# Performance work log

Hardware: AMD Instinct MI355X
Metric: run time of the kernel (lower is better)

## Reference

```python
import jax, jax.numpy as jnp
import numpy as np

E = 1024  # embed_dim
H = 16    # num_heads
D = E // H  # head_dim
B, S = 2, 2048


def setup_inputs() -> dict:
    key = jax.random.key(0)
    ks = jax.random.split(key, 8)
    q = jax.random.normal(ks[0], (B, S, E), dtype=jnp.float32)
    k = jax.random.normal(ks[1], (B, S, E), dtype=jnp.float32)
    v = jax.random.normal(ks[2], (B, S, E), dtype=jnp.float32)
    mask = jax.random.randint(ks[3], (1, 1, S, S), 0, 2, dtype=jnp.int32)
    sc = 1.0 / np.sqrt(E)
    Wqkv = jax.random.normal(ks[4], (E, 3 * E), dtype=jnp.float32) * sc  # [in, out]
    bqkv = jnp.zeros((3 * E,), dtype=jnp.float32)
    Wout = jax.random.normal(ks[5], (E, E), dtype=jnp.float32) * sc
    bout = jnp.zeros((E,), dtype=jnp.float32)
    return {"q": q, "k": k, "v": v, "mask": mask,
            "Wqkv": Wqkv, "bqkv": bqkv, "Wout": Wout, "bout": bout}


def reference(q, k, v, mask, Wqkv, bqkv, Wout, bout):
    # Fused QKV projection: project cat([q,k,v], dim=0) with the shared 3E proj,
    # then take the Q slice for q, K slice for k, V slice for v.
    x = jnp.concatenate([q, k, v], axis=0)            # [3B, S, E]
    full = jnp.einsum('bse,ef->bsf', x, Wqkv) + bqkv  # [3B, S, 3E]
    qf, kf, vf = jnp.split(full, 3, axis=0)           # each [B, S, 3E]
    qh = qf[..., :E].reshape(B, S, H, D).transpose(0, 2, 1, 3)       # [B,H,S,D]
    kh = kf[..., E:2 * E].reshape(B, S, H, D).transpose(0, 2, 1, 3)
    vh = vf[..., 2 * E:].reshape(B, S, H, D).transpose(0, 2, 1, 3)
    scores = jnp.einsum('bhqd,bhkd->bhqk', qh, kh) / np.sqrt(D)      # [B,H,S,S]
    scores = jnp.where(mask == 0, -jnp.inf, scores)
    attn = jax.nn.softmax(scores, axis=-1)
    ctx = jnp.einsum('bhqk,bhkd->bhqd', attn, vh)                    # [B,H,S,D]
    ctx = ctx.transpose(0, 2, 1, 3).reshape(B, S, E)
    return jnp.einsum('bse,ef->bsf', ctx, Wout) + bout
```

## Files before the change

kernel.cpp:

```cpp
#include <hip/hip_runtime.h>
#include <stdint.h>

#define EDIM 1024
#define HNUM 16
#define HD   64
#define BB   2
#define SS   2048
#define MTOT (BB * SS)

typedef __attribute__((ext_vector_type(8))) __bf16 bf16x8;
typedef __attribute__((ext_vector_type(8))) short short8;
typedef __attribute__((ext_vector_type(4))) short short4v;
typedef __attribute__((ext_vector_type(4))) float f32x4;

__device__ __forceinline__ short f2bf(float f) {
  union { float f; unsigned u; } x{f};
  unsigned r = (x.u + 0x7FFFu + ((x.u >> 16) & 1u)) >> 16;
  return (short)r;
}

__device__ __forceinline__ void gload16(const void* g, void* l) {
  __builtin_amdgcn_global_load_lds((const __attribute__((address_space(1))) void*)g,
                                   (__attribute__((address_space(3))) void*)l, 16, 0, 0);
}

__global__ __launch_bounds__(256) void cast_bf16(const float* __restrict__ s,
                                                 short* __restrict__ d, int n8) {
  int i = blockIdx.x * 256 + threadIdx.x;
  if (i >= n8) return;
  const float4* sp = (const float4*)s + (size_t)i * 2;
  float4 a = sp[0], b = sp[1];
  short8 r;
  r[0] = f2bf(a.x); r[1] = f2bf(a.y); r[2] = f2bf(a.z); r[3] = f2bf(a.w);
  r[4] = f2bf(b.x); r[5] = f2bf(b.y); r[6] = f2bf(b.z); r[7] = f2bf(b.w);
  *(short8*)(d + (size_t)i * 8) = r;
}

__global__ __launch_bounds__(256) void tcast(const float* __restrict__ W, int ld,
                                             int col0, short* __restrict__ D) {
  __shared__ short L[64][80];
  const int t = threadIdx.x;
  const int k0 = blockIdx.x * 64, n0 = blockIdx.y * 64;
  {
    const int kr = t >> 2, nc0 = (t & 3) * 16;
    #pragma unroll
    for (int u = 0; u < 4; ++u) {
      float4 f = *(const float4*)(W + (size_t)(k0 + kr) * ld + col0 + n0 + nc0 + u * 4);
      L[nc0 + u * 4 + 0][kr] = f2bf(f.x);
      L[nc0 + u * 4 + 1][kr] = f2bf(f.y);
      L[nc0 + u * 4 + 2][kr] = f2bf(f.z);
      L[nc0 + u * 4 + 3][kr] = f2bf(f.w);
    }
  }
  __syncthreads();
  {
    const int nr = t >> 2, kc = (t & 3) * 16;
    #pragma unroll
    for (int u = 0; u < 2; ++u) {
      short8 v = *(const short8*)&L[nr][kc + u * 8];
      *(short8*)(D + (size_t)(n0 + nr) * EDIM + k0 + kc + u * 8) = v;
    }
  }
}

__global__ __launch_bounds__(256) void pack_mask(const int* __restrict__ mask,
                                                 unsigned long long* __restrict__ pm) {
  const int wid = (blockIdx.x * 256 + threadIdx.x) >> 6;
  const int lane = threadIdx.x & 63;
  const int q = wid >> 5, kt = wid & 31;
  const int m = mask[(size_t)q * SS + kt * 64 + lane];
  const unsigned long long b = __ballot(m != 0);
  if (lane == 0) pm[(size_t)q * 32 + kt] = b;
}

template <int NFR, typename OT>
__device__ __forceinline__ void gemm_body(
    const short* __restrict__ A, const short* __restrict__ Bt,
    const float* __restrict__ bias, OT* __restrict__ O,
    int m0, int n0, int K, int N, float scale, short* As, short* Bs) {
  const int t = threadIdx.x;
  const int w = t >> 6, l = t & 63;
  const int wr = w >> 1, wc = w & 1;
  const int lr4 = l >> 4, lc = l & 15;

  f32x4 acc[4][NFR] = {};
  const int srow = t >> 3;
  const int schunk = (t & 7) ^ (srow & 7);

  for (int k0 = 0; k0 < K; k0 += 64) {
    #pragma unroll
    for (int p = 0; p < 4; ++p)
      gload16(A + (size_t)(m0 + 32 * p + srow) * K + k0 + schunk * 8,
              As + p * 2048 + w * 512);
    #pragma unroll
    for (int p = 0; p < NFR; ++p)
      gload16(Bt + (size_t)(n0 + 32 * p + srow) * K + k0 + schunk * 8,
              Bs + p * 2048 + w * 512);
    __syncthreads();

    #pragma unroll
    for (int kf = 0; kf < 2; ++kf) {
      const int c = ((4 * kf + lr4) ^ (lc & 7)) * 8;
      bf16x8 a[4], bfr[NFR];
      #pragma unroll
      for (int i = 0; i < 4; ++i)
        a[i] = *(const bf16x8*)(As + (64 * wr + 16 * i + lc) * 64 + c);
      #pragma unroll
      for (int j = 0; j < NFR; ++j)
        bfr[j] = *(const bf16x8*)(Bs + (16 * NFR * wc + 16 * j + lc) * 64 + c);
      #pragma unroll
      for (int i = 0; i < 4; ++i)
        #pragma unroll
        for (int j = 0; j < NFR; ++j)
          acc[i][j] = __builtin_amdgcn_mfma_f32_16x16x32_bf16(a[i], bfr[j], acc[i][j], 0, 0, 0);
    }
    __syncthreads();
  }

  #pragma unroll
  for (int j = 0; j < NFR; ++j) {
    const int col = n0 + 16 * NFR * wc + 16 * j + lc;
    const float bv = bias[col - n0 + n0];
    #pragma unroll
    for (int i = 0; i < 4; ++i) {
      const int rbase = m0 + 64 * wr + 16 * i + 4 * lr4;
      #pragma unroll
      for (int r = 0; r < 4; ++r) {
        float v = (acc[i][j][r] + bv) * scale;
        if constexpr (__is_same(OT, short))
          O[(size_t)(rbase + r) * N + col] = f2bf(v);
        else
          O[(size_t)(rbase + r) * N + col] = v;
      }
    }
  }
}

__global__ __launch_bounds__(256) void gemm_qkv(
    const short* __restrict__ Qb, const short* __restrict__ Kb,
    const short* __restrict__ Vb, const short* __restrict__ WqT,
    const short* __restrict__ WkT, const short* __restrict__ WvT,
    const float* __restrict__ bqkv, short* __restrict__ Qpj,
    short* __restrict__ Kpj, short* __restrict__ Vpj) {
  __shared__ short As[128 * 64];
  __shared__ short Bs[128 * 64];
  const int sel = blockIdx.y >> 3;
  const int n0 = (blockIdx.y & 7) * 128;
  const short* A  = sel == 0 ? Qb : (sel == 1 ? Kb : Vb);
  const short* Bt = sel == 0 ? WqT : (sel == 1 ? WkT : WvT);
  short* O = sel == 0 ? Qpj : (sel == 1 ? Kpj : Vpj);
  const float scale = sel == 0 ? 0.125f : 1.0f;
  gemm_body<4, short>(A, Bt, bqkv + (sel << 10), O, blockIdx.x * 128, n0,
                      EDIM, EDIM, scale, As, Bs);
}

__global__ __launch_bounds__(256) void gemm_out(
    const short* __restrict__ A, const short* __restrict__ Bt,
    const float* __restrict__ bias, float* __restrict__ O) {
  __shared__ short As[128 * 64];
  __shared__ short Bs[64 * 64];
  gemm_body<2, float>(A, Bt, bias, O, blockIdx.x * 128, blockIdx.y * 64,
                      EDIM, EDIM, 1.0f, As, Bs);
}

__global__ __launch_bounds__(256) void attn_mfma(
    const short* __restrict__ Qp, const short* __restrict__ Kp,
    const short* __restrict__ Vp, const unsigned long long* __restrict__ pmask,
    short* __restrict__ Ctx) {
  __shared__ short Ks[2][64 * 64];
  __shared__ short Vt[2][64 * 64];

  const int t = threadIdx.x, w = t >> 6, l = t & 63;
  const int lr4 = l >> 4, lc = l & 15;
  const int q0 = blockIdx.x * 64;
  const int h = blockIdx.y, b = blockIdx.z;
  const size_t hb = (size_t)b * SS * EDIM + (size_t)h * HD;
  const int qrow = q0 + 16 * w + lc;

  bf16x8 qf[2];
  #pragma unroll
  for (int kf = 0; kf < 2; ++kf)
    qf[kf] = *(const bf16x8*)(Qp + hb + (size_t)qrow * EDIM + 32 * kf + 8 * lr4);

  const int srow = t >> 3;
  const int schunk = (t & 7) ^ (srow & 7);
  const int vkey = t & 63;
  const int vdg = (t >> 6) * 16;
  const int kap = (vkey & 0x20) | ((vkey & 0xC) << 1) | ((vkey & 0x10) >> 2) | (vkey & 3);
  const int kapc = kap >> 3, kapb = kap & 7;

  #pragma unroll
  for (int p = 0; p < 2; ++p)
    gload16(Kp + hb + (size_t)(32 * p + srow) * EDIM + schunk * 8,
            &Ks[0][p * 2048 + w * 512]);
  {
    short8 v0 = *(const short8*)(Vp + hb + (size_t)vkey * EDIM + vdg);
    short8 v1 = *(const short8*)(Vp + hb + (size_t)vkey * EDIM + vdg + 8);
    #pragma unroll
    for (int e = 0; e < 8; ++e) {
      const int d0 = vdg + e, d1 = vdg + 8 + e;
      Vt[0][d0 * 64 + ((kapc ^ (d0 & 7)) << 3) + kapb] = v0[e];
      Vt[0][d1 * 64 + ((kapc ^ (d1 & 7)) << 3) + kapb] = v1[e];
    }
  }
  __syncthreads();

  f32x4 accO[4] = {};
  float mrow = -1e30f, lrow = 0.f;
  const int NT = SS / 64;

  for (int kt = 0; kt < NT; ++kt) {
    const int cur = kt & 1, nxt = cur ^ 1;
    short8 nv0, nv1;
    const bool pre = (kt + 1 < NT);
    if (pre) {
      const size_t s1 = hb + (size_t)((kt + 1) * 64) * EDIM;
      #pragma unroll
      for (int p = 0; p < 2; ++p)
        gload16(Kp + s1 + (size_t)(32 * p + srow) * EDIM + schunk * 8,
                &Ks[nxt][p * 2048 + w * 512]);
      nv0 = *(const short8*)(Vp + s1 + (size_t)vkey * EDIM + vdg);
      nv1 = *(const short8*)(Vp + s1 + (size_t)vkey * EDIM + vdg + 8);
    }
    const unsigned long long pw = pmask[(size_t)qrow * NT + kt];

    f32x4 sacc[4] = {};
    #pragma unroll
    for (int kf = 0; kf < 2; ++kf) {
      const int c = ((4 * kf + lr4) ^ (lc & 7)) * 8;
      #pragma unroll
      for (int nf = 0; nf < 4; ++nf) {
        bf16x8 kb8 = *(const bf16x8*)(&Ks[cur][(16 * nf + lc) * 64 + c]);
        sacc[nf] = __builtin_amdgcn_mfma_f32_16x16x32_bf16(kb8, qf[kf], sacc[nf], 0, 0, 0);
      }
    }

    float p[4][4];
    float mt = -1e30f;
    #pragma unroll
    for (int nf = 0; nf < 4; ++nf)
      #pragma unroll
      for (int r = 0; r < 4; ++r) {
        const float s = ((pw >> (16 * nf + 4 * lr4 + r)) & 1ull) ? sacc[nf][r] : -1e30f;
        p[nf][r] = s;
        mt = fmaxf(mt, s);
      }
    mt = fmaxf(mt, __shfl_xor(mt, 16, 64));
    mt = fmaxf(mt, __shfl_xor(mt, 32, 64));
    const float mn = fmaxf(mrow, mt);
    const float scl = __expf(mrow - mn);
    mrow = mn;
    float ls = 0.f;
    #pragma unroll
    for (int nf = 0; nf < 4; ++nf)
      #pragma unroll
      for (int r = 0; r < 4; ++r) {
        const float e = (p[nf][r] <= -1e29f) ? 0.f : __expf(p[nf][r] - mn);
        p[nf][r] = e;
        ls += e;
      }
    ls += __shfl_xor(ls, 16, 64);
    ls += __shfl_xor(ls, 32, 64);
    lrow = lrow * scl + ls;
    #pragma unroll
    for (int df = 0; df < 4; ++df)
      #pragma unroll
      for (int r = 0; r < 4; ++r)
        accO[df][r] *= scl;

    bf16x8 pf[2];
    #pragma unroll
    for (int kf = 0; kf < 2; ++kf) {
      short8 tmp;
      #pragma unroll
      for (int j = 0; j < 8; ++j)
        tmp[j] = f2bf(p[2 * kf + (j >> 2)][j & 3]);
      pf[kf] = *(bf16x8*)&tmp;
    }

    #pragma unroll
    for (int kf = 0; kf < 2; ++kf) {
      const int c = ((4 * kf + lr4) ^ (lc & 7)) * 8;
      #pragma unroll
      for (int df = 0; df < 4; ++df) {
        bf16x8 va = *(const bf16x8*)(&Vt[cur][(16 * df + lc) * 64 + c]);
        accO[df] = __builtin_amdgcn_mfma_f32_16x16x32_bf16(va, pf[kf], accO[df], 0, 0, 0);
      }
    }

    if (pre) {
      #pragma unroll
      for (int e = 0; e < 8; ++e) {
        const int d0 = vdg + e, d1 = vdg + 8 + e;
        Vt[nxt][d0 * 64 + ((kapc ^ (d0 & 7)) << 3) + kapb] = nv0[e];
        Vt[nxt][d1 * 64 + ((kapc ^ (d1 & 7)) << 3) + kapb] = nv1[e];
      }
    }
    __syncthreads();
  }

  const float inv = 1.f / lrow;
  #pragma unroll
  for (int df = 0; df < 4; ++df) {
    short4v o;
    #pragma unroll
    for (int r = 0; r < 4; ++r) o[r] = f2bf(accO[df][r] * inv);
    *(short4v*)(Ctx + hb + (size_t)qrow * EDIM + 16 * df + 4 * lr4) = o;
  }
}

extern "C" void kernel_launch(void* const* d_in, const int* in_sizes, int n_in,
                              void* d_out, int out_size, void* d_ws, size_t ws_size,
                              hipStream_t stream) {
  const float* q    = (const float*)d_in[0];
  const float* k    = (const float*)d_in[1];
  const float* v    = (const float*)d_in[2];
  const int*   mask = (const int*)d_in[3];
  const float* Wqkv = (const float*)d_in[4];
  const float* bqkv = (const float*)d_in[5];
  const float* Wout = (const float*)d_in[6];
  const float* bout = (const float*)d_in[7];
  float* out = (float*)d_out;

  const size_t mat = (size_t)MTOT * EDIM;
  const size_t wmat = (size_t)EDIM * EDIM;
  short* Qb  = (short*)d_ws;
  short* Kb  = Qb + mat;
  short* Vb  = Kb + mat;
  short* WqT = Vb + mat;
  short* WkT = WqT + wmat;
  short* WvT = WkT + wmat;
  short* WoT = WvT + wmat;
  short* Qpj = WoT + wmat;
  short* Kpj = Qpj + mat;
  short* Vpj = Kpj + mat;
  short* Ctx = Vpj + mat;
  unsigned long long* pm = (unsigned long long*)(Ctx + mat);

  const int n8 = (int)(mat / 8);
  cast_bf16<<<dim3(n8 / 256), 256, 0, stream>>>(q, Qb, n8);
  cast_bf16<<<dim3(n8 / 256), 256, 0, stream>>>(k, Kb, n8);
  cast_bf16<<<dim3(n8 / 256), 256, 0, stream>>>(v, Vb, n8);

  const dim3 tg(16, 16);
  tcast<<<tg, 256, 0, stream>>>(Wqkv, 3 * EDIM, 0,        WqT);
  tcast<<<tg, 256, 0, stream>>>(Wqkv, 3 * EDIM, EDIM,     WkT);
  tcast<<<tg, 256, 0, stream>>>(Wqkv, 3 * EDIM, 2 * EDIM, WvT);
  tcast<<<tg, 256, 0, stream>>>(Wout, EDIM,     0,        WoT);

  pack_mask<<<dim3((SS * 32 * 64) / 256), 256, 0, stream>>>(mask, pm);

  gemm_qkv<<<dim3(MTOT / 128, 24), 256, 0, stream>>>(Qb, Kb, Vb, WqT, WkT, WvT,
                                                     bqkv, Qpj, Kpj, Vpj);

  attn_mfma<<<dim3(SS / 64, HNUM, BB), 256, 0, stream>>>(Qpj, Kpj, Vpj, pm, Ctx);

  gemm_out<<<dim3(MTOT / 128, EDIM / 64), 256, 0, stream>>>(Ctx, WoT, bout, out);
}
```

Before: 315.3 us.

## Fuse prep kernels, emit pre-transposed V from QKV GEMM, lazy-rescale softmax with exp2

The eight cast, weight-transpose and mask-pack launches are merged into one prep kernel. The V projection epilogue now writes V transposed and key-permuted, so attention loads V tiles with async global-to-LDS copies instead of register transposes. The softmax folds log2(e) into the Q scale and uses exp2f, and it only rescales the accumulators when the running max grows by more than a threshold. It also applies the mask after exponentiation instead of before the max. Float-to-bf16 conversion uses the hardware cast, and the V epilogue does scattered 4-element stores.

```diff
diff --git a/kernel.cpp b/kernel.cpp
--- a/kernel.cpp
+++ b/kernel.cpp
@@ -13,10 +13,9 @@
 typedef __attribute__((ext_vector_type(4))) short short4v;
 typedef __attribute__((ext_vector_type(4))) float f32x4;
 
-__device__ __forceinline__ short f2bf(float f) {
-  union { float f; unsigned u; } x{f};
-  unsigned r = (x.u + 0x7FFFu + ((x.u >> 16) & 1u)) >> 16;
-  return (short)r;
+__device__ __forceinline__ short bfbits(float f) {
+  __bf16 h = (__bf16)f;
+  return __builtin_bit_cast(short, h);
 }
 
 __device__ __forceinline__ void gload16(const void* g, void* l) {
@@ -24,56 +23,70 @@
                                    (__attribute__((address_space(3))) void*)l, 16, 0, 0);
 }
 
-__global__ __launch_bounds__(256) void cast_bf16(const float* __restrict__ s,
-                                                 short* __restrict__ d, int n8) {
-  int i = blockIdx.x * 256 + threadIdx.x;
-  if (i >= n8) return;
-  const float4* sp = (const float4*)s + (size_t)i * 2;
-  float4 a = sp[0], b = sp[1];
-  short8 r;
-  r[0] = f2bf(a.x); r[1] = f2bf(a.y); r[2] = f2bf(a.z); r[3] = f2bf(a.w);
-  r[4] = f2bf(b.x); r[5] = f2bf(b.y); r[6] = f2bf(b.z); r[7] = f2bf(b.w);
-  *(short8*)(d + (size_t)i * 8) = r;
-}
-
-__global__ __launch_bounds__(256) void tcast(const float* __restrict__ W, int ld,
-                                             int col0, short* __restrict__ D) {
+__device__ __forceinline__ int kap_perm(int k) {
+  return (k & 0x20) | ((k & 0xC) << 1) | ((k & 0x10) >> 2) | (k & 3);
+}
+
+__global__ __launch_bounds__(256) void prep(
+    const float* __restrict__ q, const float* __restrict__ k,
+    const float* __restrict__ v, const float* __restrict__ Wqkv,
+    const float* __restrict__ Wout, const int* __restrict__ mask,
+    short* __restrict__ Qb, short* __restrict__ Kb, short* __restrict__ Vb,
+    short* __restrict__ WqT, short* __restrict__ WkT, short* __restrict__ WvT,
+    short* __restrict__ WoT, unsigned long long* __restrict__ pm) {
   __shared__ short L[64][80];
-  const int t = threadIdx.x;
-  const int k0 = blockIdx.x * 64, n0 = blockIdx.y * 64;
-  {
-    const int kr = t >> 2, nc0 = (t & 3) * 16;
-    #pragma unroll
-    for (int u = 0; u < 4; ++u) {
-      float4 f = *(const float4*)(W + (size_t)(k0 + kr) * ld + col0 + n0 + nc0 + u * 4);
-      L[nc0 + u * 4 + 0][kr] = f2bf(f.x);
-      L[nc0 + u * 4 + 1][kr] = f2bf(f.y);
-      L[nc0 + u * 4 + 2][kr] = f2bf(f.z);
-      L[nc0 + u * 4 + 3][kr] = f2bf(f.w);
-    }
-  }
-  __syncthreads();
-  {
-    const int nr = t >> 2, kc = (t & 3) * 16;
-    #pragma unroll
-    for (int u = 0; u < 2; ++u) {
-      short8 v = *(const short8*)&L[nr][kc + u * 8];
-      *(short8*)(D + (size_t)(n0 + nr) * EDIM + k0 + kc + u * 8) = v;
-    }
-  }
-}
-
-__global__ __launch_bounds__(256) void pack_mask(const int* __restrict__ mask,
-                                                 unsigned long long* __restrict__ pm) {
-  const int wid = (blockIdx.x * 256 + threadIdx.x) >> 6;
-  const int lane = threadIdx.x & 63;
-  const int q = wid >> 5, kt = wid & 31;
-  const int m = mask[(size_t)q * SS + kt * 64 + lane];
-  const unsigned long long b = __ballot(m != 0);
-  if (lane == 0) pm[(size_t)q * 32 + kt] = b;
-}
-
-template <int NFR, typename OT>
+  const int bid = blockIdx.x, t = threadIdx.x;
+
+  if (bid < 6144) {
+    const int which = bid >> 11;
+    const int i = (bid & 2047) * 256 + t;
+    const float* s = which == 0 ? q : (which == 1 ? k : v);
+    short* d = which == 0 ? Qb : (which == 1 ? Kb : Vb);
+    const float4* sp = (const float4*)s + (size_t)i * 2;
+    float4 a = sp[0], b = sp[1];
+    short8 r;
+    r[0] = bfbits(a.x); r[1] = bfbits(a.y); r[2] = bfbits(a.z); r[3] = bfbits(a.w);
+    r[4] = bfbits(b.x); r[5] = bfbits(b.y); r[6] = bfbits(b.z); r[7] = bfbits(b.w);
+    *(short8*)(d + (size_t)i * 8) = r;
+  } else if (bid < 7168) {
+    const int tb = bid - 6144;
+    const int which = tb >> 8;
+    const int k0 = ((tb >> 4) & 15) * 64, n0 = (tb & 15) * 64;
+    const float* W = which == 3 ? Wout : Wqkv;
+    const int ld = which == 3 ? EDIM : 3 * EDIM;
+    const int col0 = which == 3 ? 0 : which * EDIM;
+    short* D = which == 0 ? WqT : (which == 1 ? WkT : (which == 2 ? WvT : WoT));
+    {
+      const int kr = t >> 2, nc0 = (t & 3) * 16;
+      #pragma unroll
+      for (int u = 0; u < 4; ++u) {
+        float4 f = *(const float4*)(W + (size_t)(k0 + kr) * ld + col0 + n0 + nc0 + u * 4);
+        L[nc0 + u * 4 + 0][kr] = bfbits(f.x);
+        L[nc0 + u * 4 + 1][kr] = bfbits(f.y);
+        L[nc0 + u * 4 + 2][kr] = bfbits(f.z);
+        L[nc0 + u * 4 + 3][kr] = bfbits(f.w);
+      }
+    }
+    __syncthreads();
+    {
+      const int nr = t >> 2, kc = (t & 3) * 16;
+      #pragma unroll
+      for (int u = 0; u < 2; ++u) {
+        short8 vv = *(const short8*)&L[nr][kc + u * 8];
+        *(short8*)(D + (size_t)(n0 + nr) * EDIM + k0 + kc + u * 8) = vv;
+      }
+    }
+  } else {
+    const int wid = (bid - 7168) * 4 + (t >> 6);
+    const int lane = t & 63;
+    const int qq = wid >> 5, kt = wid & 31;
+    const int m = mask[(size_t)qq * SS + kt * 64 + lane];
+    const unsigned long long b = __ballot(m != 0);
+    if (lane == 0) pm[(size_t)qq * 32 + kt] = b;
+  }
+}
+
+template <int NFR, int MODE, typename OT>
 __device__ __forceinline__ void gemm_body(
     const short* __restrict__ A, const short* __restrict__ Bt,
     const float* __restrict__ bias, OT* __restrict__ O,
@@ -120,17 +133,27 @@
   #pragma unroll
   for (int j = 0; j < NFR; ++j) {
     const int col = n0 + 16 * NFR * wc + 16 * j + lc;
-    const float bv = bias[col - n0 + n0];
+    const float bv = bias[col];
     #pragma unroll
     for (int i = 0; i < 4; ++i) {
       const int rbase = m0 + 64 * wr + 16 * i + 4 * lr4;
-      #pragma unroll
-      for (int r = 0; r < 4; ++r) {
-        float v = (acc[i][j][r] + bv) * scale;
-        if constexpr (__is_same(OT, short))
-          O[(size_t)(rbase + r) * N + col] = f2bf(v);
-        else
-          O[(size_t)(rbase + r) * N + col] = v;
+      if constexpr (MODE == 2) {
+        const int bidx = rbase >> 11, s = rbase & 2047;
+        const int hh = col >> 6, dd = col & 63;
+        short4v o;
+        #pragma unroll
+        for (int r = 0; r < 4; ++r) o[r] = bfbits((acc[i][j][r] + bv) * scale);
+        *(short4v*)((short*)O + (((size_t)bidx * HNUM + hh) * 64 + dd) * SS +
+                    (s & ~63) + kap_perm(s & 63)) = o;
+      } else {
+        #pragma unroll
+        for (int r = 0; r < 4; ++r) {
+          float vv = (acc[i][j][r] + bv) * scale;
+          if constexpr (MODE == 0)
+            ((short*)O)[(size_t)(rbase + r) * N + col] = bfbits(vv);
+          else
+            ((float*)O)[(size_t)(rbase + r) * N + col] = vv;
+        }
       }
     }
   }
@@ -141,17 +164,21 @@
     const short* __restrict__ Vb, const short* __restrict__ WqT,
     const short* __restrict__ WkT, const short* __restrict__ WvT,
     const float* __restrict__ bqkv, short* __restrict__ Qpj,
-    short* __restrict__ Kpj, short* __restrict__ Vpj) {
+    short* __restrict__ Kpj, short* __restrict__ VT) {
   __shared__ short As[128 * 64];
   __shared__ short Bs[128 * 64];
   const int sel = blockIdx.y >> 3;
   const int n0 = (blockIdx.y & 7) * 128;
-  const short* A  = sel == 0 ? Qb : (sel == 1 ? Kb : Vb);
-  const short* Bt = sel == 0 ? WqT : (sel == 1 ? WkT : WvT);
-  short* O = sel == 0 ? Qpj : (sel == 1 ? Kpj : Vpj);
-  const float scale = sel == 0 ? 0.125f : 1.0f;
-  gemm_body<4, short>(A, Bt, bqkv + (sel << 10), O, blockIdx.x * 128, n0,
-                      EDIM, EDIM, scale, As, Bs);
+  const int m0 = blockIdx.x * 128;
+  if (sel == 0)
+    gemm_body<4, 0, short>(Qb, WqT, bqkv, Qpj, m0, n0, EDIM, EDIM,
+                           0.125f * 1.44269504089f, As, Bs);
+  else if (sel == 1)
+    gemm_body<4, 0, short>(Kb, WkT, bqkv + EDIM, Kpj, m0, n0, EDIM, EDIM,
+                           1.0f, As, Bs);
+  else
+    gemm_body<4, 2, short>(Vb, WvT, bqkv + 2 * EDIM, VT, m0, n0, EDIM, EDIM,
+                           1.0f, As, Bs);
 }
 
 __global__ __launch_bounds__(256) void gemm_out(
@@ -159,13 +186,13 @@
     const float* __restrict__ bias, float* __restrict__ O) {
   __shared__ short As[128 * 64];
   __shared__ short Bs[64 * 64];
-  gemm_body<2, float>(A, Bt, bias, O, blockIdx.x * 128, blockIdx.y * 64,
-                      EDIM, EDIM, 1.0f, As, Bs);
+  gemm_body<2, 1, float>(A, Bt, bias, O, blockIdx.x * 128, blockIdx.y * 64,
+                         EDIM, EDIM, 1.0f, As, Bs);
 }
 
 __global__ __launch_bounds__(256) void attn_mfma(
     const short* __restrict__ Qp, const short* __restrict__ Kp,
-    const short* __restrict__ Vp, const unsigned long long* __restrict__ pmask,
+    const short* __restrict__ VT, const unsigned long long* __restrict__ pmask,
     short* __restrict__ Ctx) {
   __shared__ short Ks[2][64 * 64];
   __shared__ short Vt[2][64 * 64];
@@ -175,6 +202,7 @@
   const int q0 = blockIdx.x * 64;
   const int h = blockIdx.y, b = blockIdx.z;
   const size_t hb = (size_t)b * SS * EDIM + (size_t)h * HD;
+  const size_t hv = ((size_t)b * HNUM + h) * 64 * SS;
   const int qrow = q0 + 16 * w + lc;
 
   bf16x8 qf[2];
@@ -184,24 +212,13 @@
 
   const int srow = t >> 3;
   const int schunk = (t & 7) ^ (srow & 7);
-  const int vkey = t & 63;
-  const int vdg = (t >> 6) * 16;
-  const int kap = (vkey & 0x20) | ((vkey & 0xC) << 1) | ((vkey & 0x10) >> 2) | (vkey & 3);
-  const int kapc = kap >> 3, kapb = kap & 7;
 
   #pragma unroll
-  for (int p = 0; p < 2; ++p)
+  for (int p = 0; p < 2; ++p) {
     gload16(Kp + hb + (size_t)(32 * p + srow) * EDIM + schunk * 8,
             &Ks[0][p * 2048 + w * 512]);
-  {
-    short8 v0 = *(const short8*)(Vp + hb + (size_t)vkey * EDIM + vdg);
-    short8 v1 = *(const short8*)(Vp + hb + (size_t)vkey * EDIM + vdg + 8);
-    #pragma unroll
-    for (int e = 0; e < 8; ++e) {
-      const int d0 = vdg + e, d1 = vdg + 8 + e;
-      Vt[0][d0 * 64 + ((kapc ^ (d0 & 7)) << 3) + kapb] = v0[e];
-      Vt[0][d1 * 64 + ((kapc ^ (d1 & 7)) << 3) + kapb] = v1[e];
-    }
+    gload16(VT + hv + (size_t)(32 * p + srow) * SS + schunk * 8,
+            &Vt[0][p * 2048 + w * 512]);
   }
   __syncthreads();
 
@@ -211,18 +228,18 @@
 
   for (int kt = 0; kt < NT; ++kt) {
     const int cur = kt & 1, nxt = cur ^ 1;
-    short8 nv0, nv1;
-    const bool pre = (kt + 1 < NT);
-    if (pre) {
-      const size_t s1 = hb + (size_t)((kt + 1) * 64) * EDIM;
-      #pragma unroll
-      for (int p = 0; p < 2; ++p)
-        gload16(Kp + s1 + (size_t)(32 * p + srow) * EDIM + schunk * 8,
+    const unsigned long long pw = pmask[(size_t)qrow * NT + kt];
+    if (kt + 1 < NT) {
+      const size_t sK = hb + (size_t)((kt + 1) * 64) * EDIM;
+      const size_t sV = hv + (size_t)((kt + 1) * 64);
+      #pragma unroll
+      for (int p = 0; p < 2; ++p) {
+        gload16(Kp + sK + (size_t)(32 * p + srow) * EDIM + schunk * 8,
                 &Ks[nxt][p * 2048 + w * 512]);
-      nv0 = *(const short8*)(Vp + s1 + (size_t)vkey * EDIM + vdg);
-      nv1 = *(const short8*)(Vp + s1 + (size_t)vkey * EDIM + vdg + 8);
-    }
-    const unsigned long long pw = pmask[(size_t)qrow * NT + kt];
+        gload16(VT + sV + (size_t)(32 * p + srow) * SS + schunk * 8,
+                &Vt[nxt][p * 2048 + w * 512]);
+      }
+    }
 
     f32x4 sacc[4] = {};
     #pragma unroll
@@ -235,48 +252,43 @@
       }
     }
 
-    float p[4][4];
     float mt = -1e30f;
     #pragma unroll
     for (int nf = 0; nf < 4; ++nf)
       #pragma unroll
-      for (int r = 0; r < 4; ++r) {
-        const float s = ((pw >> (16 * nf + 4 * lr4 + r)) & 1ull) ? sacc[nf][r] : -1e30f;
-        p[nf][r] = s;
-        mt = fmaxf(mt, s);
-      }
+      for (int r = 0; r < 4; ++r)
+        mt = fmaxf(mt, sacc[nf][r]);
     mt = fmaxf(mt, __shfl_xor(mt, 16, 64));
     mt = fmaxf(mt, __shfl_xor(mt, 32, 64));
-    const float mn = fmaxf(mrow, mt);
-    const float scl = __expf(mrow - mn);
-    mrow = mn;
+
+    if (__any(mt > mrow + 7.0f)) {
+      const float mn = fmaxf(mrow, mt);
+      const float scl = exp2f(mrow - mn);
+      mrow = mn;
+      lrow *= scl;
+      #pragma unroll
+      for (int df = 0; df < 4; ++df)
+        #pragma unroll
+        for (int r = 0; r < 4; ++r)
+          accO[df][r] *= scl;
+    }
+
     float ls = 0.f;
-    #pragma unroll
-    for (int nf = 0; nf < 4; ++nf)
+    bf16x8 pf[2];
+    #pragma unroll
+    for (int nf = 0; nf < 4; ++nf) {
+      const unsigned nib = (unsigned)(pw >> (16 * nf + 4 * lr4)) & 15u;
       #pragma unroll
       for (int r = 0; r < 4; ++r) {
-        const float e = (p[nf][r] <= -1e29f) ? 0.f : __expf(p[nf][r] - mn);
-        p[nf][r] = e;
-        ls += e;
-      }
+        const float e = exp2f(sacc[nf][r] - mrow);
+        const float p = (nib >> r) & 1u ? e : 0.f;
+        ls += p;
+        pf[nf >> 1][4 * (nf & 1) + r] = (__bf16)p;
+      }
+    }
     ls += __shfl_xor(ls, 16, 64);
     ls += __shfl_xor(ls, 32, 64);
-    lrow = lrow * scl + ls;
-    #pragma unroll
-    for (int df = 0; df < 4; ++df)
-      #pragma unroll
-      for (int r = 0; r < 4; ++r)
-        accO[df][r] *= scl;
-
-    bf16x8 pf[2];
-    #pragma unroll
-    for (int kf = 0; kf < 2; ++kf) {
-      short8 tmp;
-      #pragma unroll
-      for (int j = 0; j < 8; ++j)
-        tmp[j] = f2bf(p[2 * kf + (j >> 2)][j & 3]);
-      pf[kf] = *(bf16x8*)&tmp;
-    }
+    lrow += ls;
 
     #pragma unroll
     for (int kf = 0; kf < 2; ++kf) {
@@ -285,15 +297,6 @@
       for (int df = 0; df < 4; ++df) {
         bf16x8 va = *(const bf16x8*)(&Vt[cur][(16 * df + lc) * 64 + c]);
         accO[df] = __builtin_amdgcn_mfma_f32_16x16x32_bf16(va, pf[kf], accO[df], 0, 0, 0);
-      }
-    }
-
-    if (pre) {
-      #pragma unroll
-      for (int e = 0; e < 8; ++e) {
-        const int d0 = vdg + e, d1 = vdg + 8 + e;
-        Vt[nxt][d0 * 64 + ((kapc ^ (d0 & 7)) << 3) + kapb] = nv0[e];
-        Vt[nxt][d1 * 64 + ((kapc ^ (d1 & 7)) << 3) + kapb] = nv1[e];
       }
     }
     __syncthreads();
@@ -304,7 +307,7 @@
   for (int df = 0; df < 4; ++df) {
     short4v o;
     #pragma unroll
-    for (int r = 0; r < 4; ++r) o[r] = f2bf(accO[df][r] * inv);
+    for (int r = 0; r < 4; ++r) o[r] = bfbits(accO[df][r] * inv);
     *(short4v*)(Ctx + hb + (size_t)qrow * EDIM + 16 * df + 4 * lr4) = o;
   }
 }
@@ -333,27 +336,17 @@
   short* WoT = WvT + wmat;
   short* Qpj = WoT + wmat;
   short* Kpj = Qpj + mat;
-  short* Vpj = Kpj + mat;
-  short* Ctx = Vpj + mat;
+  short* VT  = Kpj + mat;
+  short* Ctx = VT + mat;
   unsigned long long* pm = (unsigned long long*)(Ctx + mat);
 
-  const int n8 = (int)(mat / 8);
-  cast_bf16<<<dim3(n8 / 256), 256, 0, stream>>>(q, Qb, n8);
-  cast_bf16<<<dim3(n8 / 256), 256, 0, stream>>>(k, Kb, n8);
-  cast_bf16<<<dim3(n8 / 256), 256, 0, stream>>>(v, Vb, n8);
-
-  const dim3 tg(16, 16);
-  tcast<<<tg, 256, 0, stream>>>(Wqkv, 3 * EDIM, 0,        WqT);
-  tcast<<<tg, 256, 0, stream>>>(Wqkv, 3 * EDIM, EDIM,     WkT);
-  tcast<<<tg, 256, 0, stream>>>(Wqkv, 3 * EDIM, 2 * EDIM, WvT);
-  tcast<<<tg, 256, 0, stream>>>(Wout, EDIM,     0,        WoT);
-
-  pack_mask<<<dim3((SS * 32 * 64) / 256), 256, 0, stream>>>(mask, pm);
+  prep<<<dim3(23552), 256, 0, stream>>>(q, k, v, Wqkv, Wout, mask,
+                                        Qb, Kb, Vb, WqT, WkT, WvT, WoT, pm);
 
   gemm_qkv<<<dim3(MTOT / 128, 24), 256, 0, stream>>>(Qb, Kb, Vb, WqT, WkT, WvT,
-                                                     bqkv, Qpj, Kpj, Vpj);
-
-  attn_mfma<<<dim3(SS / 64, HNUM, BB), 256, 0, stream>>>(Qpj, Kpj, Vpj, pm, Ctx);
+                                                     bqkv, Qpj, Kpj, VT);
+
+  attn_mfma<<<dim3(SS / 64, HNUM, BB), 256, 0, stream>>>(Qpj, Kpj, VT, pm, Ctx);
 
   gemm_out<<<dim3(MTOT / 128, EDIM / 64), 256, 0, stream>>>(Ctx, WoT, bout, out);
 }
```

After: 267.8 us. -15.1%, faster.
